# Optimization experiments

Measured on AMD Instinct MI355X. Metric: run time of the kernel, lower is better.

Reference implementation:

```python
import jax, jax.numpy as jnp
import numpy as np

B, S, D, H = 2, 2048, 1024, 16
DK = D // H
BASE = 10000.0

def setup_inputs() -> dict:
    key = jax.random.key(0)
    k1, k2, k3 = jax.random.split(key, 3)
    hidden_states = jax.random.normal(k1, (B, S, D), dtype=jnp.float32)
    position_ids = jnp.tile(jnp.arange(S, dtype=jnp.int32)[None, :], (B, 1))
    c_attn_w = jax.random.normal(k2, (D, 3 * D), dtype=jnp.float32) * 0.02
    c_attn_b = jnp.zeros((3 * D,), dtype=jnp.float32)
    c_proj_w = jax.random.normal(k3, (D, D), dtype=jnp.float32) * 0.02
    c_proj_b = jnp.zeros((D,), dtype=jnp.float32)
    return {"hidden_states": hidden_states, "position_ids": position_ids,
            "c_attn_w": c_attn_w, "c_attn_b": c_attn_b,
            "c_proj_w": c_proj_w, "c_proj_b": c_proj_b}

def rotate_half(x):
    x1, x2 = x[..., : x.shape[-1] // 2], x[..., x.shape[-1] // 2 :]
    return jnp.concatenate((-x2, x1), axis=-1)

def reference(hidden_states, position_ids, c_attn_w, c_attn_b, c_proj_w, c_proj_b):
    b, s, d = hidden_states.shape
    # QKV projection (Conv1D == linear with [in, out] weight)
    qkv = hidden_states @ c_attn_w + c_attn_b            # [B,S,3D]
    q, k, v = jnp.split(qkv, 3, axis=-1)
    def heads(x):
        return x.reshape(b, s, H, DK).transpose(0, 2, 1, 3)  # [B,H,S,dk]
    q, k, v = heads(q), heads(k), heads(v)
    # rotary embedding
    inv_freq = 1.0 / (BASE ** (jnp.arange(0, DK, 2, dtype=jnp.float32) / DK))
    freqs = position_ids.astype(jnp.float32)[:, :, None] * inv_freq[None, None, :]  # [B,S,dk/2]
    emb = jnp.concatenate((freqs, freqs), axis=-1)       # [B,S,dk]
    cos = jnp.cos(emb)[:, None, :, :]                    # [B,1,S,dk]
    sin = jnp.sin(emb)[:, None, :, :]
    q = q * cos + rotate_half(q) * sin
    k = k * cos + rotate_half(k) * sin
    # scores in fp32 (matches baddbmm under autocast disabled)
    scale = 1.0 / jnp.sqrt(jnp.float32(DK))
    w = jnp.einsum('bhqd,bhkd->bhqk', q.astype(jnp.float32), k.astype(jnp.float32)) * scale
    causal = jnp.tril(jnp.ones((s, s), dtype=bool))
    w = jnp.where(causal[None, None], w, jnp.finfo(w.dtype).min)
    w = jax.nn.softmax(w, axis=-1).astype(v.dtype)
    out = jnp.einsum('bhqk,bhkd->bhqd', w, v)            # [B,H,S,dk]
    out = out.transpose(0, 2, 1, 3).reshape(b, s, d)     # merge heads
    return out @ c_proj_w + c_proj_b
```

## Files before the change

### kernel.cpp

```cpp
#include <hip/hip_runtime.h>
#include <hip/hip_bf16.h>
#include <cstdint>
#include <math.h>

#define NB   2
#define NS   2048
#define ND   1024
#define NH   16
#define NDK  64
#define N3D  3072

typedef __attribute__((ext_vector_type(8))) short short8;
typedef __attribute__((ext_vector_type(4))) float f32x4;

__device__ __forceinline__ unsigned short f2bf_u(float f) {
  __hip_bfloat16 h = __float2bfloat16(f);
  return __builtin_bit_cast(unsigned short, h);
}
__device__ __forceinline__ float bfu2f(unsigned short u) {
  __hip_bfloat16 h = __builtin_bit_cast(__hip_bfloat16, u);
  return __bfloat162float(h);
}
__device__ __forceinline__ float bfr(float x) {
  return __bfloat162float(__float2bfloat16(x));
}

#define MFMA16(a, b, c) __builtin_amdgcn_mfma_f32_16x16x32_bf16((a), (b), (c), 0, 0, 0)
#define AS1 __attribute__((address_space(1)))
#define AS3 __attribute__((address_space(3)))

__global__ void trig_tab(const int* __restrict__ pos, float* __restrict__ ctab,
                         float* __restrict__ stab) {
  const int idx = blockIdx.x * 256 + threadIdx.x;
  const int d = idx & 31;
  const int s = (idx >> 5) & (NS - 1);
  const int b = idx >> 16;
  const float p   = (float)pos[b * NS + s];
  const float pw  = (float)pow(10000.0, (double)d / 32.0);
  const float inv = __fdiv_rn(1.0f, pw);
  const float ang = __fmul_rn(p, inv);
  ctab[idx] = (float)cos((double)ang);
  stab[idx] = (float)sin((double)ang);
}

__global__ void cvt_bf16(const float* __restrict__ src, unsigned short* __restrict__ dst, int n4) {
  const int i = blockIdx.x * 256 + threadIdx.x;
  if (i >= n4) return;
  float4 v = reinterpret_cast<const float4*>(src)[i];
  ushort4 o;
  o.x = f2bf_u(v.x); o.y = f2bf_u(v.y); o.z = f2bf_u(v.z); o.w = f2bf_u(v.w);
  reinterpret_cast<ushort4*>(dst)[i] = o;
}

__global__ void transpose_cvt(const float* __restrict__ src, unsigned short* __restrict__ dst,
                              int R, int srcStride) {
  __shared__ float tile[32][33];
  int c0 = blockIdx.x * 32, r0 = blockIdx.y * 32;
  int tx = threadIdx.x, ty = threadIdx.y;
  #pragma unroll
  for (int i = 0; i < 32; i += 8)
    tile[ty + i][tx] = src[(size_t)(r0 + ty + i) * srcStride + (c0 + tx)];
  __syncthreads();
  #pragma unroll
  for (int i = 0; i < 32; i += 8)
    dst[(size_t)(c0 + ty + i) * R + (r0 + tx)] = f2bf_u(tile[tx][ty + i]);
}

template<int MODE>
__global__ __launch_bounds__(256, 2)
void gemm2(const unsigned short* __restrict__ A16, const unsigned short* __restrict__ BT, int K,
           const float* __restrict__ bias, const float* __restrict__ ctab,
           const float* __restrict__ stab, unsigned short* __restrict__ qcb,
           unsigned short* __restrict__ kcb, unsigned short* __restrict__ vT,
           float* __restrict__ fout) {
  __shared__ unsigned short As[128 * 64];
  __shared__ unsigned short Bs[128 * 64];
  const int tid = threadIdx.x;
  const int wave = tid >> 6;
  const int lane = tid & 63;
  const int m0 = blockIdx.x * 128;
  const int n0 = blockIdx.y * 128;
  const int wr = wave >> 1, wc = wave & 1;

  f32x4 acc[4][4] = {};

  for (int kt = 0; kt < K; kt += 64) {
    __syncthreads();
    #pragma unroll
    for (int j = 0; j < 4; ++j) {
      const int c = (wave * 4 + j) * 64 + lane;
      const int row = c >> 3, col8 = c & 7;
      __builtin_amdgcn_global_load_lds(
          (const AS1 void*)(A16 + (size_t)(m0 + row) * K + kt + col8 * 8),
          (AS3 void*)(As + (wave * 4 + j) * 512), 16, 0, 0);
    }
    #pragma unroll
    for (int j = 0; j < 4; ++j) {
      const int c = (wave * 4 + j) * 64 + lane;
      const int row = c >> 3, col8 = c & 7;
      __builtin_amdgcn_global_load_lds(
          (const AS1 void*)(BT + (size_t)(n0 + row) * K + kt + col8 * 8),
          (AS3 void*)(Bs + (wave * 4 + j) * 512), 16, 0, 0);
    }
    asm volatile("s_waitcnt vmcnt(0)" ::: "memory");
    __syncthreads();

    #pragma unroll
    for (int kc = 0; kc < 2; ++kc) {
      short8 af[4], bfrg[4];
      const int gw = kc * 4 + (lane >> 4);
      #pragma unroll
      for (int m = 0; m < 4; ++m) {
        const int row = wr * 64 + m * 16 + (lane & 15);
        af[m] = *reinterpret_cast<const short8*>(As + row * 64 + gw * 8);
      }
      #pragma unroll
      for (int n = 0; n < 4; ++n) {
        const int row = wc * 64 + n * 16 + (lane & 15);
        bfrg[n] = *reinterpret_cast<const short8*>(Bs + row * 64 + gw * 8);
      }
      #pragma unroll
      for (int m = 0; m < 4; ++m)
        #pragma unroll
        for (int n = 0; n < 4; ++n)
          acc[m][n] = MFMA16(af[m], bfrg[n], acc[m][n]);
    }
  }

  const int colbase = n0 + wc * 64;
  const int rowbase = m0 + wr * 64;

  if (MODE == 1) {
    #pragma unroll
    for (int n = 0; n < 4; ++n) {
      const int col = colbase + n * 16 + (lane & 15);
      const float bv = bfr(bias[col]);
      #pragma unroll
      for (int m = 0; m < 4; ++m)
        #pragma unroll
        for (int jj = 0; jj < 4; ++jj) {
          const int row = rowbase + m * 16 + (lane >> 4) * 4 + jj;
          float r = bfr(acc[m][n][jj]);
          r = bfr(r + bv);
          fout[(size_t)row * ND + col] = r;
        }
    }
    return;
  }

  const int sec = colbase >> 10;
  if (sec < 2) {
    unsigned short* dst = (sec == 0) ? qcb : kcb;
    #pragma unroll
    for (int n = 0; n < 2; ++n) {
      const int col1 = colbase + n * 16 + (lane & 15);
      const int col2 = col1 + 32;
      const float bv1 = bfr(bias[col1]);
      const float bv2 = bfr(bias[col2]);
      const int h = (col1 & 1023) >> 6;
      const int d = col1 & 63;
      #pragma unroll
      for (int m = 0; m < 4; ++m)
        #pragma unroll
        for (int jj = 0; jj < 4; ++jj) {
          const int row = rowbase + m * 16 + (lane >> 4) * 4 + jj;
          const int b = row >> 11, s = row & (NS - 1);
          const float x1 = bfr(bfr(acc[m][n][jj])     + bv1);
          const float x2 = bfr(bfr(acc[m][n + 2][jj]) + bv2);
          const float cs = ctab[(size_t)(b * NS + s) * 32 + d];
          const float sn = stab[(size_t)(b * NS + s) * 32 + d];
          const size_t base = ((size_t)(b * NH + h) * NS + s) * NDK + d;
          dst[base]      = f2bf_u(__fadd_rn(__fmul_rn(x1, cs), __fmul_rn(-x2, sn)));
          dst[base + 32] = f2bf_u(__fadd_rn(__fmul_rn(x2, cs), __fmul_rn(x1, sn)));
        }
    }
  } else {
    #pragma unroll
    for (int n = 0; n < 4; ++n) {
      const int col = colbase + n * 16 + (lane & 15);
      const int lc = col & 1023;
      const int h = lc >> 6, dk = lc & 63;
      const float bv = bfr(bias[col]);
      #pragma unroll
      for (int m = 0; m < 4; ++m)
        #pragma unroll
        for (int jj = 0; jj < 4; ++jj) {
          const int row = rowbase + m * 16 + (lane >> 4) * 4 + jj;
          const int b = row >> 11, s = row & (NS - 1);
          float r = bfr(acc[m][n][jj]);
          r = bfr(r + bv);
          vT[((size_t)(b * NH + h) * NDK + dk) * NS + s] = f2bf_u(r);
        }
    }
  }
}

__global__ __launch_bounds__(256, 4)
void flash6(const unsigned short* __restrict__ qc, const unsigned short* __restrict__ kc,
            const unsigned short* __restrict__ vT, unsigned short* __restrict__ aob) {
  __shared__ unsigned short Ks[2][64 * 64];
  __shared__ unsigned short Vs[2][64 * 64];
  __shared__ unsigned short Pl[4][16 * 64];
  const int tid = threadIdx.x;
  const int wave = tid >> 6, lane = tid & 63;
  const int flat = blockIdx.x;
  const int xcd = flat & 7;
  const int idx = flat >> 3;
  const int hg = idx >> 4;
  const int i4 = idx & 15;
  const int bh = xcd * 4 + hg;
  const int b = bh >> 4, h = bh & 15;
  const unsigned short* Qh = qc + (size_t)bh * NS * NDK;
  const unsigned short* Kh = kc + (size_t)bh * NS * NDK;
  const unsigned short* Vh = vT + (size_t)bh * NDK * NS;
  const short8 vone = {0x3F80, 0x3F80, 0x3F80, 0x3F80, 0x3F80, 0x3F80, 0x3F80, 0x3F80};

#define STAGE_K(KV0, BUF)                                                          \
  {                                                                                \
    _Pragma("unroll")                                                              \
    for (int j = 0; j < 2; ++j) {                                                  \
      const int c = (j * 4 + wave) * 64 + lane;                                    \
      const int row = c >> 3, ch = c & 7;                                          \
      __builtin_amdgcn_global_load_lds(                                            \
          (const AS1 void*)(Kh + (size_t)((KV0) + row) * NDK + ((ch ^ (row & 7)) * 8)), \
          (AS3 void*)((BUF) + (j * 4 + wave) * 512), 16, 0, 0);                    \
    }                                                                              \
  }
#define STAGE_V(KV0, BUF)                                                          \
  {                                                                                \
    _Pragma("unroll")                                                              \
    for (int j = 0; j < 2; ++j) {                                                  \
      const int c = (j * 4 + wave) * 64 + lane;                                    \
      const int row = c >> 3, ch = c & 7;                                          \
      __builtin_amdgcn_global_load_lds(                                            \
          (const AS1 void*)(Vh + (size_t)row * NS + (KV0) + ((ch ^ (row & 7)) * 8)), \
          (AS3 void*)((BUF) + (j * 4 + wave) * 512), 16, 0, 0);                    \
    }                                                                              \
  }

  for (int qi = 0; qi < 2; ++qi) {
    const int qt = (qi == 0) ? (31 - i4) : i4;
    const int qw = qt * 64 + wave * 16;

    short8 aq[2];
    {
      const int qrow = qw + (lane & 15);
      #pragma unroll
      for (int kk = 0; kk < 2; ++kk)
        aq[kk] = *reinterpret_cast<const short8*>(Qh + (size_t)qrow * NDK + kk * 32 + (lane >> 4) * 8);
    }

    const int ntiles = qt + 1;
    int cur = 0;
    STAGE_K(0, Ks[0]);
    STAGE_V(0, Vs[0]);
    asm volatile("s_waitcnt vmcnt(0)" ::: "memory");
    __syncthreads();

    f32x4 oacc[4] = {};
    f32x4 lacc = {};

    for (int t = 0; t < ntiles; ++t) {
      const int kv0 = t * 64;
      if (t + 1 < ntiles) {
        STAGE_K(kv0 + 64, Ks[cur ^ 1]);
        STAGE_V(kv0 + 64, Vs[cur ^ 1]);
      }

      f32x4 sacc[4];
      #pragma unroll
      for (int n = 0; n < 4; ++n) {
        const int krow = n * 16 + (lane & 15);
        f32x4 z = {};
        #pragma unroll
        for (int kk = 0; kk < 2; ++kk) {
          const int gw = kk * 4 + (lane >> 4);
          short8 bk = *reinterpret_cast<const short8*>(Ks[cur] + krow * 64 + ((gw ^ (krow & 7)) * 8));
          z = MFMA16(aq[kk], bk, z);
        }
        sacc[n] = z;
      }
      const bool diag = (t == qt);
      #pragma unroll
      for (int n = 0; n < 4; ++n)
        #pragma unroll
        for (int jj = 0; jj < 4; ++jj) {
          float sv = sacc[n][jj] * 0.125f - 8.0f;
          if (diag) {
            const int col = kv0 + n * 16 + (lane & 15);
            const int row = qw + (lane >> 4) * 4 + jj;
            if (col > row) sv = -1e30f;
          }
          const float e = __expf(sv);
          const int prow = (lane >> 4) * 4 + jj;
          const int pcol = n * 16 + (lane & 15);
          const int chunk = pcol >> 3;
          Pl[wave][prow * 64 + (chunk ^ (prow & 7)) * 8 + (pcol & 7)] = f2bf_u(e);
        }

      short8 pa[2];
      #pragma unroll
      for (int kk = 0; kk < 2; ++kk) {
        const int prow = lane & 15;
        const int gw = kk * 4 + (lane >> 4);
        pa[kk] = *reinterpret_cast<const short8*>(Pl[wave] + prow * 64 + ((gw ^ (prow & 7)) * 8));
      }
      #pragma unroll
      for (int n2 = 0; n2 < 4; ++n2) {
        const int dk = n2 * 16 + (lane & 15);
        #pragma unroll
        for (int kk = 0; kk < 2; ++kk) {
          const int gw = kk * 4 + (lane >> 4);
          short8 bv = *reinterpret_cast<const short8*>(Vs[cur] + dk * 64 + ((gw ^ (dk & 7)) * 8));
          oacc[n2] = MFMA16(pa[kk], bv, oacc[n2]);
        }
      }
      #pragma unroll
      for (int kk = 0; kk < 2; ++kk)
        lacc = MFMA16(pa[kk], vone, lacc);

      asm volatile("s_waitcnt vmcnt(0)" ::: "memory");
      __syncthreads();
      cur ^= 1;
    }

    #pragma unroll
    for (int n2 = 0; n2 < 4; ++n2)
      #pragma unroll
      for (int jj = 0; jj < 4; ++jj) {
        const int row = qw + (lane >> 4) * 4 + jj;
        aob[(size_t)(b * NS + row) * ND + h * NDK + n2 * 16 + (lane & 15)] =
            f2bf_u(oacc[n2][jj] / lacc[jj]);
      }
  }
#undef STAGE_K
#undef STAGE_V
}

extern "C" void kernel_launch(void* const* d_in, const int* in_sizes, int n_in,
                              void* d_out, int out_size, void* d_ws, size_t ws_size,
                              hipStream_t stream) {
  const float* hs     = (const float*)d_in[0];
  const int*   pos    = (const int*)d_in[1];
  const float* w_attn = (const float*)d_in[2];
  const float* b_attn = (const float*)d_in[3];
  const float* w_proj = (const float*)d_in[4];
  const float* b_proj = (const float*)d_in[5];
  float* out = (float*)d_out;

  char* ws = (char*)d_ws;
  unsigned short* qc     = (unsigned short*)(ws);
  unsigned short* kcb    = (unsigned short*)(ws + (8ull  << 20));
  unsigned short* vT     = (unsigned short*)(ws + (16ull << 20));
  unsigned short* wqkvT  = (unsigned short*)(ws + (24ull << 20));
  unsigned short* aob    = (unsigned short*)(ws + (24ull << 20));
  unsigned short* wprojT = (unsigned short*)(ws + (32ull << 20));
  float*          ctab   = (float*)(ws + (34ull << 20));
  float*          stab   = (float*)(ws + (34ull << 20) + (512ull << 10));

  unsigned short* hsb = (unsigned short*)d_out;

  trig_tab<<<(NB * NS * 32) / 256, 256, 0, stream>>>(pos, ctab, stab);
  cvt_bf16<<<(NB * NS * ND / 4 + 255) / 256, 256, 0, stream>>>(hs, hsb, NB * NS * ND / 4);
  transpose_cvt<<<dim3(96, 32), dim3(32, 8), 0, stream>>>(w_attn, wqkvT, ND, N3D);
  gemm2<0><<<dim3(32, 24), 256, 0, stream>>>(hsb, wqkvT, ND, b_attn, ctab, stab,
                                             qc, kcb, vT, nullptr);
  flash6<<<512, 256, 0, stream>>>(qc, kcb, vT, aob);
  transpose_cvt<<<dim3(32, 32), dim3(32, 8), 0, stream>>>(w_proj, wprojT, ND, ND);
  gemm2<1><<<dim3(32, 8), 256, 0, stream>>>(aob, wprojT, ND, b_proj, nullptr, nullptr,
                                            nullptr, nullptr, nullptr, out);
}
```

Baseline: 121.3 us.

## Software-pipeline flash attention: defer P·V of previous tile behind next QK^T

Restructures the attention inner loop so each iteration first does the P·V MFMAs for the previous tile, then computes QK^T and the exp for the current tile. This needs a double-buffered P scratch and a triple-buffered V tile in LDS. The aim is to overlap the exp/softmax ALU work with matrix-core work and shorten the dependency chain within each iteration. Launch bounds drop from 4 to 2 blocks per CU, and the extra LDS plus a trailing sync may lower occupancy.

```diff
diff --git a/kernel.cpp b/kernel.cpp
--- a/kernel.cpp
+++ b/kernel.cpp
@@ -195,12 +195,12 @@
   }
 }
 
-__global__ __launch_bounds__(256, 4)
-void flash6(const unsigned short* __restrict__ qc, const unsigned short* __restrict__ kc,
+__global__ __launch_bounds__(256, 2)
+void flash7(const unsigned short* __restrict__ qc, const unsigned short* __restrict__ kc,
             const unsigned short* __restrict__ vT, unsigned short* __restrict__ aob) {
   __shared__ unsigned short Ks[2][64 * 64];
-  __shared__ unsigned short Vs[2][64 * 64];
-  __shared__ unsigned short Pl[4][16 * 64];
+  __shared__ unsigned short Vs[3][64 * 64];
+  __shared__ unsigned short Pl[4][2][16 * 64];
   const int tid = threadIdx.x;
   const int wave = tid >> 6, lane = tid & 63;
   const int flat = blockIdx.x;
@@ -238,6 +238,32 @@
     }                                                                              \
   }
 
+#define PV_TILE(VB, PPB)                                                           \
+  {                                                                                \
+    short8 pa[2];                                                                  \
+    _Pragma("unroll")                                                              \
+    for (int kk = 0; kk < 2; ++kk) {                                               \
+      const int prow = lane & 15;                                                  \
+      const int gw = kk * 4 + (lane >> 4);                                         \
+      pa[kk] = *reinterpret_cast<const short8*>(Pl[wave][PPB] + prow * 64 +        \
+                                                ((gw ^ (prow & 7)) * 8));          \
+    }                                                                              \
+    _Pragma("unroll")                                                              \
+    for (int n2 = 0; n2 < 4; ++n2) {                                               \
+      const int dk = n2 * 16 + (lane & 15);                                        \
+      _Pragma("unroll")                                                            \
+      for (int kk = 0; kk < 2; ++kk) {                                             \
+        const int gw = kk * 4 + (lane >> 4);                                       \
+        short8 bv = *reinterpret_cast<const short8*>(Vs[VB] + dk * 64 +            \
+                                                     ((gw ^ (dk & 7)) * 8));       \
+        oacc[n2] = MFMA16(pa[kk], bv, oacc[n2]);                                   \
+      }                                                                            \
+    }                                                                              \
+    _Pragma("unroll")                                                              \
+    for (int kk = 0; kk < 2; ++kk)                                                 \
+      lacc = MFMA16(pa[kk], vone, lacc);                                           \
+  }
+
   for (int qi = 0; qi < 2; ++qi) {
     const int qt = (qi == 0) ? (31 - i4) : i4;
     const int qw = qt * 64 + wave * 16;
@@ -251,7 +277,6 @@
     }
 
     const int ntiles = qt + 1;
-    int cur = 0;
     STAGE_K(0, Ks[0]);
     STAGE_V(0, Vs[0]);
     asm volatile("s_waitcnt vmcnt(0)" ::: "memory");
@@ -259,12 +284,15 @@
 
     f32x4 oacc[4] = {};
     f32x4 lacc = {};
+    int pb = 0;
+    int vprev = 2, vcurr = 0, vnext = 1;
 
     for (int t = 0; t < ntiles; ++t) {
-      const int kv0 = t * 64;
+      if (t > 0) PV_TILE(vprev, pb ^ 1);
+
       if (t + 1 < ntiles) {
-        STAGE_K(kv0 + 64, Ks[cur ^ 1]);
-        STAGE_V(kv0 + 64, Vs[cur ^ 1]);
+        STAGE_K(t * 64 + 64, Ks[(t + 1) & 1]);
+        STAGE_V(t * 64 + 64, Vs[vnext]);
       }
 
       f32x4 sacc[4];
@@ -275,12 +303,13 @@
         #pragma unroll
         for (int kk = 0; kk < 2; ++kk) {
           const int gw = kk * 4 + (lane >> 4);
-          short8 bk = *reinterpret_cast<const short8*>(Ks[cur] + krow * 64 + ((gw ^ (krow & 7)) * 8));
+          short8 bk = *reinterpret_cast<const short8*>(Ks[t & 1] + krow * 64 + ((gw ^ (krow & 7)) * 8));
           z = MFMA16(aq[kk], bk, z);
         }
         sacc[n] = z;
       }
       const bool diag = (t == qt);
+      const int kv0 = t * 64;
       #pragma unroll
       for (int n = 0; n < 4; ++n)
         #pragma unroll
@@ -295,34 +324,16 @@
           const int prow = (lane >> 4) * 4 + jj;
           const int pcol = n * 16 + (lane & 15);
           const int chunk = pcol >> 3;
-          Pl[wave][prow * 64 + (chunk ^ (prow & 7)) * 8 + (pcol & 7)] = f2bf_u(e);
-        }
-
-      short8 pa[2];
-      #pragma unroll
-      for (int kk = 0; kk < 2; ++kk) {
-        const int prow = lane & 15;
-        const int gw = kk * 4 + (lane >> 4);
-        pa[kk] = *reinterpret_cast<const short8*>(Pl[wave] + prow * 64 + ((gw ^ (prow & 7)) * 8));
-      }
-      #pragma unroll
-      for (int n2 = 0; n2 < 4; ++n2) {
-        const int dk = n2 * 16 + (lane & 15);
-        #pragma unroll
-        for (int kk = 0; kk < 2; ++kk) {
-          const int gw = kk * 4 + (lane >> 4);
-          short8 bv = *reinterpret_cast<const short8*>(Vs[cur] + dk * 64 + ((gw ^ (dk & 7)) * 8));
-          oacc[n2] = MFMA16(pa[kk], bv, oacc[n2]);
-        }
-      }
-      #pragma unroll
-      for (int kk = 0; kk < 2; ++kk)
-        lacc = MFMA16(pa[kk], vone, lacc);
+          Pl[wave][pb][prow * 64 + (chunk ^ (prow & 7)) * 8 + (pcol & 7)] = f2bf_u(e);
+        }
 
       asm volatile("s_waitcnt vmcnt(0)" ::: "memory");
       __syncthreads();
-      cur ^= 1;
-    }
+      pb ^= 1;
+      vprev = vcurr; vcurr = vnext; vnext = (vnext == 2) ? 0 : vnext + 1;
+    }
+
+    PV_TILE(vprev, pb ^ 1);
 
     #pragma unroll
     for (int n2 = 0; n2 < 4; ++n2)
@@ -332,9 +343,12 @@
         aob[(size_t)(b * NS + row) * ND + h * NDK + n2 * 16 + (lane & 15)] =
             f2bf_u(oacc[n2][jj] / lacc[jj]);
       }
+
+    __syncthreads();
   }
 #undef STAGE_K
 #undef STAGE_V
+#undef PV_TILE
 }
 
 extern "C" void kernel_launch(void* const* d_in, const int* in_sizes, int n_in,
@@ -365,7 +379,7 @@
   transpose_cvt<<<dim3(96, 32), dim3(32, 8), 0, stream>>>(w_attn, wqkvT, ND, N3D);
   gemm2<0><<<dim3(32, 24), 256, 0, stream>>>(hsb, wqkvT, ND, b_attn, ctab, stab,
                                              qc, kcb, vT, nullptr);
-  flash6<<<512, 256, 0, stream>>>(qc, kcb, vT, aob);
+  flash7<<<512, 256, 0, stream>>>(qc, kcb, vT, aob);
   transpose_cvt<<<dim3(32, 32), dim3(32, 8), 0, stream>>>(w_proj, wprojT, ND, ND);
   gemm2<1><<<dim3(32, 8), 256, 0, stream>>>(aob, wprojT, ND, b_proj, nullptr, nullptr,
                                             nullptr, nullptr, nullptr, out);
```

Result: no change. 122.0 us (+0.5%).
